# Kernel optimization log

Hardware: AMD Instinct MI355X
Metric: run time of the kernel (lower is better)

## Reference

```python
import jax, jax.numpy as jnp
import numpy as np

B, T, C = 4, 2048, 1024   # batch, seq (block_size), n_embd
H, D = 16, 64             # num_heads, head_size (H*D == C)


def setup_inputs() -> dict:
    key = jax.random.key(0)
    ks = jax.random.split(key, 6)
    s = 0.02
    return {
        "x":  jax.random.normal(ks[0], (B, T, C), jnp.float32),
        "Wq": jax.random.normal(ks[1], (H, C, D), jnp.float32) * s,
        "Wk": jax.random.normal(ks[2], (H, C, D), jnp.float32) * s,
        "Wv": jax.random.normal(ks[3], (H, C, D), jnp.float32) * s,
        "Wp": jax.random.normal(ks[4], (C, C), jnp.float32) * s,
        "bp": jnp.zeros((C,), jnp.float32),
        "is_masked": 1,
    }


def reference(x, Wq, Wk, Wv, Wp, bp, is_masked):
    # Batched per-head projections (original loops over H separate Linears)
    q = jnp.einsum("btc,hcd->bhtd", x, Wq)
    k = jnp.einsum("btc,hcd->bhtd", x, Wk)
    v = jnp.einsum("btc,hcd->bhtd", x, Wv)
    # NOTE: original divides by sqrt(C) where C = n_embd (input dim), not head_size
    scores = jnp.einsum("bhtd,bhsd->bhts", q, k) / jnp.sqrt(jnp.asarray(C, x.dtype))
    if is_masked:
        causal = jnp.tril(jnp.ones((T, T), bool))
        scores = jnp.where(causal, scores, jnp.asarray(-jnp.inf, scores.dtype))
    attn = jax.nn.softmax(scores, axis=-1)   # dropout is identity in eval mode
    out = jnp.einsum("bhts,bhsd->bhtd", attn, v)
    # concat heads along the last dim: [B,T,H*D] == [B,T,C]
    out = out.transpose(0, 2, 1, 3).reshape(B, T, C)
    return out @ Wp.T + bp
```

## Files before the change

kernel.cpp:

```cpp
#include <hip/hip_runtime.h>
#include <stdint.h>
#include <type_traits>

typedef unsigned short u16;
typedef unsigned int u32;
typedef __attribute__((ext_vector_type(8))) short frag8;
typedef __attribute__((ext_vector_type(4))) float fx4;
typedef __attribute__((ext_vector_type(16))) float fx16;

#define MFMA(a, b, c) __builtin_amdgcn_mfma_f32_16x16x32_bf16((a), (b), (c), 0, 0, 0)
#define MFMA32(a, b, c) __builtin_amdgcn_mfma_f32_32x32x16_bf16((a), (b), (c), 0, 0, 0)

__device__ __forceinline__ void gload16(const void* g, void* l) {
  __builtin_amdgcn_global_load_lds((const __attribute__((address_space(1))) void*)g,
                                   (__attribute__((address_space(3))) void*)l, 16, 0, 0);
}

__device__ __forceinline__ u16 f2bf(float f) {
  union { float f; unsigned int u; } c; c.f = f;
  unsigned int r = c.u + 0x7FFFu + ((c.u >> 16) & 1u);
  return (u16)(r >> 16);
}

__device__ __forceinline__ u32 cvtpk(float lo, float hi) {
  u32 r;
  asm("v_cvt_pk_bf16_f32 %0, %1, %2" : "=v"(r) : "v"(lo), "v"(hi));
  return r;
}


__global__ __launch_bounds__(256) void cvt_x(const float* __restrict__ x, u16* __restrict__ xb) {
  const int n4 = (8192 * 1024) / 4;
  for (int i = blockIdx.x * 256 + threadIdx.x; i < n4; i += 2048 * 256) {
    float4 v = ((const float4*)x)[i];
    ushort4 o;
    o.x = f2bf(v.x); o.y = f2bf(v.y); o.z = f2bf(v.z); o.w = f2bf(v.w);
    ((ushort4*)xb)[i] = o;
  }
}

__global__ __launch_bounds__(256) void cvt_wqkv(const float* __restrict__ Wq,
                                                const float* __restrict__ Wk,
                                                const float* __restrict__ Wv,
                                                u16* __restrict__ Wt) {
  __shared__ u16 Tls[64][72];
  int hh = blockIdx.x;
  int c0 = blockIdx.y * 64;
  int type = hh >> 4, h = hh & 15;
  const float* Wsrc = (type == 0 ? Wq : (type == 1 ? Wk : Wv)) + (size_t)h * 1024 * 64;
  int t = threadIdx.x;
  int cr = t >> 4, q4 = (t & 15) * 4;
  for (int i = 0; i < 4; ++i) {
    int c = cr + i * 16;
    float4 v = *(const float4*)(Wsrc + (size_t)(c0 + c) * 64 + q4);
    Tls[q4 + 0][c] = f2bf(v.x);
    Tls[q4 + 1][c] = f2bf(v.y);
    Tls[q4 + 2][c] = f2bf(v.z);
    Tls[q4 + 3][c] = f2bf(v.w);
  }
  __syncthreads();
  for (int i = 0; i < 4; ++i) {
    int d = cr + i * 16;
    ushort4 o;
    o.x = Tls[d][q4 + 0]; o.y = Tls[d][q4 + 1]; o.z = Tls[d][q4 + 2]; o.w = Tls[d][q4 + 3];
    *(ushort4*)(Wt + ((size_t)hh * 64 + d) * 1024 + c0 + q4) = o;
  }
}

__global__ __launch_bounds__(256) void cvt_wp(const float* __restrict__ Wp, u16* __restrict__ wb) {
  const int n4 = (1024 * 1024) / 4;
  for (int i = blockIdx.x * 256 + threadIdx.x; i < n4; i += 1024 * 256) {
    float4 v = ((const float4*)Wp)[i];
    ushort4 o;
    o.x = f2bf(v.x); o.y = f2bf(v.y); o.z = f2bf(v.z); o.w = f2bf(v.w);
    ((ushort4*)wb)[i] = o;
  }
}

__global__ __launch_bounds__(256) void transpose_v(const u16* __restrict__ Vb, u16* __restrict__ VTg) {
  __shared__ u16 T[64 * 64];
  int bh = blockIdx.x, t0 = blockIdx.y * 64;
  const u16* src = Vb + ((size_t)bh * 2048 + t0) * 64;
  int tid = threadIdx.x;
  int tl = tid >> 2, c16 = (tid & 3) * 16;
  int swzw = (tl & 7) << 4;
  frag8 a = *(const frag8*)(src + (size_t)tl * 64 + c16);
  frag8 b = *(const frag8*)(src + (size_t)tl * 64 + c16 + 8);
  *(frag8*)((char*)T + tl * 128 + ((c16 * 2) ^ swzw)) = a;
  *(frag8*)((char*)T + tl * 128 + ((c16 * 2 + 16) ^ swzw)) = b;
  __syncthreads();
  int d_ = tid & 63;
#pragma unroll
  for (int k = 0; k < 2; ++k) {
    int c_ = (tid >> 6) + 4 * k;
    frag8 o;
#pragma unroll
    for (int j = 0; j < 8; ++j) {
      int t = c_ * 8 + j;
      o[j] = *(const u16*)((const char*)T + t * 128 + ((2 * d_) ^ ((t & 7) << 4)));
    }
    *(frag8*)(VTg + ((size_t)bh * 64 + d_) * 2048 + t0 + c_ * 8) = o;
  }
}


template <int BN, int MODE>
__global__ __launch_bounds__(512, 2) void gemm2(const u16* __restrict__ A, const u16* __restrict__ Bw,
                                                u16* __restrict__ Qb, u16* __restrict__ Kb,
                                                u16* __restrict__ Vb, float* __restrict__ outp,
                                                const float* __restrict__ bp) {
  constexpr int NI = BN / 64;
  constexpr int NB = BN / 64;
  constexpr int BBYTES = BN * 128;
  __shared__ __align__(16) char LDSC[65536 + 3 * BBYTES];
  const int tid = threadIdx.x, w = tid >> 6, lane = tid & 63;
  const int lr = lane & 15, lg = lane >> 4;
  constexpr int NBY = (BN == 192) ? 16 : 8;
  const int wg = blockIdx.x;
  const int xcd = wg & 7, loc = wg >> 3;
  const int bx = xcd * 4 + loc / NBY;
  const int by = loc % NBY;
  const int m0 = bx * 256, n0 = by * BN;
  const int r8 = lane >> 3;
  const int c8 = ((lane & 7) ^ r8) * 8;
  const u16* aS[4];
  const u16* bS[NB];
#pragma unroll
  for (int l = 0; l < 4; ++l) aS[l] = A + (size_t)(m0 + l * 64 + w * 8 + r8) * 1024 + c8;
#pragma unroll
  for (int l = 0; l < NB; ++l) bS[l] = Bw + (size_t)(n0 + l * 64 + w * 8 + r8) * 1024 + c8;
  const int wmB = (w >> 2) * 128, wnB = (w & 3) * (BN / 4);

  auto rdA = [&](const char* ab, int mi, int ks) -> frag8 {
    int row = wmB + mi * 16 + lr;
    return *(const frag8*)(ab + row * 128 + ((((ks << 2) + lg) ^ (lr & 7)) << 4));
  };
  auto rdB = [&](const char* bbuf, int ni, int ks) -> frag8 {
    int row = wnB + ni * 16 + lr;
    return *(const frag8*)(bbuf + row * 128 + ((((ks << 2) + lg) ^ (lr & 7)) << 4));
  };

  fx4 acc[8][NI] = {};

#pragma unroll
  for (int l = 0; l < 4; ++l) gload16(aS[l], LDSC + l * 8192 + w * 1024);
#pragma unroll
  for (int l = 0; l < NB; ++l) gload16(bS[l], LDSC + 65536 + l * 8192 + w * 1024);
#pragma unroll
  for (int l = 0; l < NB; ++l) gload16(bS[l] + 64, LDSC + 65536 + BBYTES + l * 8192 + w * 1024);
  if constexpr (NB == 3) asm volatile("s_waitcnt vmcnt(3)" ::: "memory");
  else asm volatile("s_waitcnt vmcnt(2)" ::: "memory");
  __builtin_amdgcn_s_barrier();

  for (int t = 0; t < 16; ++t) {
    const char* ab = LDSC + (t & 1) * 32768;
    const char* bb = LDSC + 65536 + (t % 3) * BBYTES;
    char* abN = LDSC + ((t + 1) & 1) * 32768;
    char* bbN = LDSC + 65536 + ((t + 2) % 3) * BBYTES;
    frag8 bfr[NI][2];
#pragma unroll
    for (int q = 0; q < 4; ++q) {
      if (q == 0) {
#pragma unroll
        for (int ni = 0; ni < NI; ++ni) {
          bfr[ni][0] = rdB(bb, ni, 0);
          bfr[ni][1] = rdB(bb, ni, 1);
        }
      }
      frag8 a00 = rdA(ab, 2 * q + 0, 0), a01 = rdA(ab, 2 * q + 0, 1);
      frag8 a10 = rdA(ab, 2 * q + 1, 0), a11 = rdA(ab, 2 * q + 1, 1);
      if (q == 0 && t + 1 < 16) {
#pragma unroll
        for (int l = 0; l < 4; ++l) gload16(aS[l] + (t + 1) * 64, abN + l * 8192 + w * 1024);
      }
      if (q == 2 && t + 2 < 16) {
        gload16(bS[0] + (t + 2) * 64, bbN + 0 * 8192 + w * 1024);
        gload16(bS[1] + (t + 2) * 64, bbN + 1 * 8192 + w * 1024);
      }
      if (q == 3 && t + 2 < 16 && NB == 3) {
        gload16(bS[2] + (t + 2) * 64, bbN + 2 * 8192 + w * 1024);
      }
      __builtin_amdgcn_s_barrier();
      __builtin_amdgcn_s_setprio(1);
#pragma unroll
      for (int ni = 0; ni < NI; ++ni) {
        acc[2 * q + 0][ni] = MFMA(a00, bfr[ni][0], acc[2 * q + 0][ni]);
        acc[2 * q + 0][ni] = MFMA(a01, bfr[ni][1], acc[2 * q + 0][ni]);
        acc[2 * q + 1][ni] = MFMA(a10, bfr[ni][0], acc[2 * q + 1][ni]);
        acc[2 * q + 1][ni] = MFMA(a11, bfr[ni][1], acc[2 * q + 1][ni]);
      }
      __builtin_amdgcn_s_setprio(0);
      if (q == 3) {
        if (t < 14) {
          if constexpr (NB == 3) asm volatile("s_waitcnt vmcnt(3)" ::: "memory");
          else asm volatile("s_waitcnt vmcnt(2)" ::: "memory");
        } else {
          asm volatile("s_waitcnt vmcnt(0)" ::: "memory");
        }
      }
      __builtin_amdgcn_s_barrier();
    }
  }

#pragma unroll
  for (int mi = 0; mi < 8; ++mi)
#pragma unroll
    for (int r = 0; r < 4; ++r) {
      int m = m0 + wmB + mi * 16 + lg * 4 + r;
      if (MODE == 0) {
        int b = m >> 11, tt = m & 2047;
#pragma unroll
        for (int ni = 0; ni < NI; ++ni) {
          int n = n0 + wnB + ni * 16 + lr;
          int type = n >> 10, h = (n >> 6) & 15, d = n & 63;
          u16* dst = (type == 0) ? Qb : ((type == 1) ? Kb : Vb);
          float v = acc[mi][ni][r];
          if (type == 0) v *= 0.04508422002778011f;
          dst[((size_t)(b * 16 + h) * 2048 + tt) * 64 + d] = f2bf(v);
        }
      } else {
#pragma unroll
        for (int ni = 0; ni < NI; ++ni) {
          int n = n0 + wnB + ni * 16 + lr;
          outp[(size_t)m * 1024 + n] = acc[mi][ni][r] + bp[n];
        }
      }
    }
}


__global__ __launch_bounds__(256, 4) void attn(const u16* __restrict__ Qb, const u16* __restrict__ Kb,
                                               const u16* __restrict__ VTg, u16* __restrict__ Ao,
                                               const int* __restrict__ mflag) {
  __shared__ __align__(16) char LDS[32768];
  const int tid = threadIdx.x, w = tid >> 6, lane = tid & 63;
  const int l31 = lane & 31, hi = lane >> 5;
  const int bh = blockIdx.x;
  const int qt = 15 - (int)blockIdx.y;
  const int masked = mflag[0];
  const int qbase = qt * 128;
  const u16* Qh = Qb + (size_t)bh * (2048 * 64);
  const u16* Kh = Kb + (size_t)bh * (2048 * 64);
  const u16* Vh = VTg + (size_t)bh * (64 * 2048);
  const int qrow = qbase + w * 32 + l31;
  frag8 qf[4];
#pragma unroll
  for (int s = 0; s < 4; ++s) qf[s] = *(const frag8*)(Qh + (size_t)qrow * 64 + s * 16 + hi * 8);
  const int srow = lane >> 3;
  const int schunk = ((lane & 7) ^ srow) * 8;
  const int c0 = w * 2, c1 = w * 2 + 1;
  const u16* kg0 = Kh + (size_t)(c0 * 8 + srow) * 64 + schunk;
  const u16* kg1 = Kh + (size_t)(c1 * 8 + srow) * 64 + schunk;
  const u16* vg0 = Vh + (size_t)(c0 * 8 + srow) * 2048 + schunk;
  const u16* vg1 = Vh + (size_t)(c1 * 8 + srow) * 2048 + schunk;
  const int aK = l31 * 128 + ((hi * 16) ^ ((l31 & 7) << 4));
  const int qmax_w = qbase + w * 32 + 31;
  const int qmin_w = qbase + w * 32;
  float m_run = -__builtin_inff(), l_run = 0.f;
  fx16 oa0 = {}, oa1 = {};
  const int nt = masked ? (2 * qt + 2) : 32;

  auto STAGE = [&](int B, int T) {
    size_t ko = (size_t)T * 4096, vo = (size_t)T * 64;
    gload16(kg0 + ko, LDS + B * 8192 + c0 * 1024);
    gload16(kg1 + ko, LDS + B * 8192 + c1 * 1024);
    gload16(vg0 + vo, LDS + 16384 + B * 8192 + c0 * 1024);
    gload16(vg1 + vo, LDS + 16384 + B * 8192 + c1 * 1024);
  };

  auto TILE = [&](auto Bc, int T) {
    constexpr int B = decltype(Bc)::value;
    if (T + 1 < nt) STAGE(B ^ 1, T + 1);
    bool act = (!masked) || (T * 64 <= qmax_w);
    if (act) {
      fx16 s0v = {}, s1v = {};
#pragma unroll
      for (int ds = 0; ds < 4; ++ds) {
        frag8 k0 = *(const frag8*)(LDS + B * 8192 + (aK ^ (ds << 5)));
        frag8 k1 = *(const frag8*)(LDS + B * 8192 + 4096 + (aK ^ (ds << 5)));
        s0v = MFMA32(k0, qf[ds], s0v);
        s1v = MFMA32(k1, qf[ds], s1v);
      }
      if (masked && T * 64 + 63 > qmin_w) {
#pragma unroll
        for (int g = 0; g < 4; ++g)
#pragma unroll
          for (int r = 0; r < 4; ++r) {
            int sg = T * 64 + r + 8 * g + 4 * hi;
            if (sg > qrow) s0v[4 * g + r] = -__builtin_inff();
            if (sg + 32 > qrow) s1v[4 * g + r] = -__builtin_inff();
          }
      }
      float mx = s0v[0];
#pragma unroll
      for (int i = 1; i < 16; ++i) mx = fmaxf(mx, s0v[i]);
#pragma unroll
      for (int i = 0; i < 16; ++i) mx = fmaxf(mx, s1v[i]);
      mx = fmaxf(mx, __int_as_float(__shfl_xor(__float_as_int(mx), 32)));
      if (!__all(mx <= m_run + 8.0f)) {
        float mn = fmaxf(m_run, mx);
        float al = __builtin_amdgcn_exp2f(m_run - mn);
#pragma unroll
        for (int i = 0; i < 16; ++i) { oa0[i] *= al; oa1[i] *= al; }
        l_run *= al;
        m_run = mn;
      }
      float ps = 0.f;
#pragma unroll
      for (int i = 0; i < 16; ++i) {
        s0v[i] = __builtin_amdgcn_exp2f(s0v[i] - m_run); ps += s0v[i];
      }
#pragma unroll
      for (int i = 0; i < 16; ++i) {
        s1v[i] = __builtin_amdgcn_exp2f(s1v[i] - m_run); ps += s1v[i];
      }
      ps += __int_as_float(__shfl_xor(__float_as_int(ps), 32));
      l_run += ps;
#pragma unroll
      for (int kt = 0; kt < 4; ++kt) {
        const int b8 = (kt & 1) * 8;
        float p0, p1, p2, p3, p4, p5, p6, p7;
        if (kt < 2) { p0=s0v[b8+0];p1=s0v[b8+1];p2=s0v[b8+2];p3=s0v[b8+3];p4=s0v[b8+4];p5=s0v[b8+5];p6=s0v[b8+6];p7=s0v[b8+7]; }
        else        { p0=s1v[b8+0];p1=s1v[b8+1];p2=s1v[b8+2];p3=s1v[b8+3];p4=s1v[b8+4];p5=s1v[b8+5];p6=s1v[b8+6];p7=s1v[b8+7]; }
        u32 X0 = cvtpk(p0, p1), X1 = cvtpk(p2, p3);
        u32 Y0 = cvtpk(p4, p5), Y1 = cvtpk(p6, p7);
        u32 sel0 = hi ? X0 : Y0, sel1 = hi ? X1 : Y1;
        u32 got0 = (u32)__shfl_xor((int)sel0, 32);
        u32 got1 = (u32)__shfl_xor((int)sel1, 32);
        union { u32 u[4]; frag8 f; } pf;
        pf.u[0] = hi ? got0 : X0;
        pf.u[1] = hi ? got1 : X1;
        pf.u[2] = hi ? Y0 : got0;
        pf.u[3] = hi ? Y1 : got1;
        frag8 v0 = *(const frag8*)(LDS + 16384 + B * 8192 + (aK ^ (kt << 5)));
        frag8 v1 = *(const frag8*)(LDS + 16384 + B * 8192 + 4096 + (aK ^ (kt << 5)));
        oa0 = MFMA32(v0, pf.f, oa0);
        oa1 = MFMA32(v1, pf.f, oa1);
      }
    }
    asm volatile("s_waitcnt vmcnt(0)" ::: "memory");
    __builtin_amdgcn_s_barrier();
  };

  STAGE(0, 0);
  asm volatile("s_waitcnt vmcnt(0)" ::: "memory");
  __builtin_amdgcn_s_barrier();
  int t = 0;
  while (true) {
    TILE(std::integral_constant<int, 0>{}, t); ++t; if (t >= nt) break;
    TILE(std::integral_constant<int, 1>{}, t); ++t; if (t >= nt) break;
  }

  float inv = 1.0f / l_run;
  int b = bh >> 4, hh = bh & 15;
  u16* orow = Ao + ((size_t)b * 2048 + qrow) * 1024 + hh * 64;
#pragma unroll
  for (int g = 0; g < 4; ++g) {
    int d0 = 8 * g + 4 * hi;
    u32 wA = cvtpk(oa0[4 * g + 0] * inv, oa0[4 * g + 1] * inv);
    u32 wB = cvtpk(oa0[4 * g + 2] * inv, oa0[4 * g + 3] * inv);
    u32 wC = cvtpk(oa1[4 * g + 0] * inv, oa1[4 * g + 1] * inv);
    u32 wD = cvtpk(oa1[4 * g + 2] * inv, oa1[4 * g + 3] * inv);
    *(u32*)(orow + d0 + 0) = wA;
    *(u32*)(orow + d0 + 2) = wB;
    *(u32*)(orow + d0 + 32) = wC;
    *(u32*)(orow + d0 + 34) = wD;
  }
}


extern "C" void kernel_launch(void* const* d_in, const int* in_sizes, int n_in,
                              void* d_out, int out_size, void* d_ws, size_t ws_size,
                              hipStream_t stream) {
  const float* x = (const float*)d_in[0];
  const float* Wq = (const float*)d_in[1];
  const float* Wk = (const float*)d_in[2];
  const float* Wv = (const float*)d_in[3];
  const float* Wp = (const float*)d_in[4];
  const float* bp = (const float*)d_in[5];
  const int* is_masked = (const int*)d_in[6];
  float* out = (float*)d_out;
  char* ws = (char*)d_ws;
  u16* Xbf = (u16*)(ws + 0);
  u16* Wt  = (u16*)(ws + 16777216);
  u16* Wpb = (u16*)(ws + 23068672);
  u16* Qb  = (u16*)(ws + 25165824);
  u16* Kb  = (u16*)(ws + 41943040);
  u16* Vb  = (u16*)(ws + 58720256);
  u16* Ao  = (u16*)(ws + 75497472);
  u16* VTg = Xbf;

  cvt_x<<<2048, 256, 0, stream>>>(x, Xbf);
  cvt_wqkv<<<dim3(48, 16), 256, 0, stream>>>(Wq, Wk, Wv, Wt);
  cvt_wp<<<1024, 256, 0, stream>>>(Wp, Wpb);
  gemm2<192, 0><<<512, 512, 0, stream>>>(Xbf, Wt, Qb, Kb, Vb, nullptr, nullptr);
  transpose_v<<<dim3(64, 32), 256, 0, stream>>>(Vb, VTg);
  attn<<<dim3(64, 16), 256, 0, stream>>>(Qb, Kb, VTg, Ao, is_masked);
  gemm2<128, 1><<<256, 512, 0, stream>>>(Ao, Wpb, nullptr, nullptr, nullptr, out, bp);
}
```

Measured before the change: 161.2 us.

## Retile GEMM warps to 4x2 layout, single barrier per k-step, tree reductions in softmax

The projection GEMM changes its warp layout from 2x4 (128 rows per warp) to 4x2 (64 rows by BN/2 columns per warp). Each k-step now issues all of its global-to-LDS prefetches up front, software-pipelines the A-fragment reads across the m loop, and uses one barrier per k-step instead of eight. Launch bounds drop to one block per SM to allow more registers. In the attention kernel, the row max and sum reductions become balanced trees to shorten dependency chains. The trade-off is lower occupancy in exchange for fewer barriers and better instruction-level parallelism.

```diff
diff --git a/kernel.cpp b/kernel.cpp
--- a/kernel.cpp
+++ b/kernel.cpp
@@ -26,6 +26,10 @@
   u32 r;
   asm("v_cvt_pk_bf16_f32 %0, %1, %2" : "=v"(r) : "v"(lo), "v"(hi));
   return r;
+}
+
+__device__ __forceinline__ float fmax3(float a, float b, float c) {
+  return fmaxf(fmaxf(a, b), c);
 }
 
 
@@ -105,11 +109,11 @@
 
 
 template <int BN, int MODE>
-__global__ __launch_bounds__(512, 2) void gemm2(const u16* __restrict__ A, const u16* __restrict__ Bw,
+__global__ __launch_bounds__(512, 1) void gemm2(const u16* __restrict__ A, const u16* __restrict__ Bw,
                                                 u16* __restrict__ Qb, u16* __restrict__ Kb,
                                                 u16* __restrict__ Vb, float* __restrict__ outp,
                                                 const float* __restrict__ bp) {
-  constexpr int NI = BN / 64;
+  constexpr int NI = BN / 32;
   constexpr int NB = BN / 64;
   constexpr int BBYTES = BN * 128;
   __shared__ __align__(16) char LDSC[65536 + 3 * BBYTES];
@@ -129,7 +133,7 @@
   for (int l = 0; l < 4; ++l) aS[l] = A + (size_t)(m0 + l * 64 + w * 8 + r8) * 1024 + c8;
 #pragma unroll
   for (int l = 0; l < NB; ++l) bS[l] = Bw + (size_t)(n0 + l * 64 + w * 8 + r8) * 1024 + c8;
-  const int wmB = (w >> 2) * 128, wnB = (w & 3) * (BN / 4);
+  const int wmB = (w >> 1) * 64, wnB = (w & 1) * (BN / 2);
 
   auto rdA = [&](const char* ab, int mi, int ks) -> frag8 {
     int row = wmB + mi * 16 + lr;
@@ -140,7 +144,7 @@
     return *(const frag8*)(bbuf + row * 128 + ((((ks << 2) + lg) ^ (lr & 7)) << 4));
   };
 
-  fx4 acc[8][NI] = {};
+  fx4 acc[4][NI] = {};
 
 #pragma unroll
   for (int l = 0; l < 4; ++l) gload16(aS[l], LDSC + l * 8192 + w * 1024);
@@ -157,53 +161,47 @@
     const char* bb = LDSC + 65536 + (t % 3) * BBYTES;
     char* abN = LDSC + ((t + 1) & 1) * 32768;
     char* bbN = LDSC + 65536 + ((t + 2) % 3) * BBYTES;
-    frag8 bfr[NI][2];
-#pragma unroll
-    for (int q = 0; q < 4; ++q) {
-      if (q == 0) {
-#pragma unroll
-        for (int ni = 0; ni < NI; ++ni) {
-          bfr[ni][0] = rdB(bb, ni, 0);
-          bfr[ni][1] = rdB(bb, ni, 1);
-        }
-      }
-      frag8 a00 = rdA(ab, 2 * q + 0, 0), a01 = rdA(ab, 2 * q + 0, 1);
-      frag8 a10 = rdA(ab, 2 * q + 1, 0), a11 = rdA(ab, 2 * q + 1, 1);
-      if (q == 0 && t + 1 < 16) {
-#pragma unroll
-        for (int l = 0; l < 4; ++l) gload16(aS[l] + (t + 1) * 64, abN + l * 8192 + w * 1024);
-      }
-      if (q == 2 && t + 2 < 16) {
-        gload16(bS[0] + (t + 2) * 64, bbN + 0 * 8192 + w * 1024);
-        gload16(bS[1] + (t + 2) * 64, bbN + 1 * 8192 + w * 1024);
-      }
-      if (q == 3 && t + 2 < 16 && NB == 3) {
-        gload16(bS[2] + (t + 2) * 64, bbN + 2 * 8192 + w * 1024);
-      }
-      __builtin_amdgcn_s_barrier();
+    if (t + 1 < 16) {
+#pragma unroll
+      for (int l = 0; l < 4; ++l) gload16(aS[l] + (t + 1) * 64, abN + l * 8192 + w * 1024);
+    }
+    if (t + 2 < 16) {
+#pragma unroll
+      for (int l = 0; l < NB; ++l) gload16(bS[l] + (t + 2) * 64, bbN + l * 8192 + w * 1024);
+    }
+    frag8 Bf[NI][2];
+#pragma unroll
+    for (int ni = 0; ni < NI; ++ni) {
+      Bf[ni][0] = rdB(bb, ni, 0);
+      Bf[ni][1] = rdB(bb, ni, 1);
+    }
+    frag8 a0 = rdA(ab, 0, 0), a1 = rdA(ab, 0, 1);
+#pragma unroll
+    for (int mi = 0; mi < 4; ++mi) {
+      frag8 c0 = a0, c1 = a1;
+      if (mi < 3) {
+        a0 = rdA(ab, mi + 1, 0);
+        a1 = rdA(ab, mi + 1, 1);
+      }
       __builtin_amdgcn_s_setprio(1);
 #pragma unroll
       for (int ni = 0; ni < NI; ++ni) {
-        acc[2 * q + 0][ni] = MFMA(a00, bfr[ni][0], acc[2 * q + 0][ni]);
-        acc[2 * q + 0][ni] = MFMA(a01, bfr[ni][1], acc[2 * q + 0][ni]);
-        acc[2 * q + 1][ni] = MFMA(a10, bfr[ni][0], acc[2 * q + 1][ni]);
-        acc[2 * q + 1][ni] = MFMA(a11, bfr[ni][1], acc[2 * q + 1][ni]);
+        acc[mi][ni] = MFMA(c0, Bf[ni][0], acc[mi][ni]);
+        acc[mi][ni] = MFMA(c1, Bf[ni][1], acc[mi][ni]);
       }
       __builtin_amdgcn_s_setprio(0);
-      if (q == 3) {
-        if (t < 14) {
-          if constexpr (NB == 3) asm volatile("s_waitcnt vmcnt(3)" ::: "memory");
-          else asm volatile("s_waitcnt vmcnt(2)" ::: "memory");
-        } else {
-          asm volatile("s_waitcnt vmcnt(0)" ::: "memory");
-        }
-      }
-      __builtin_amdgcn_s_barrier();
-    }
-  }
-
-#pragma unroll
-  for (int mi = 0; mi < 8; ++mi)
+    }
+    if (t < 14) {
+      if constexpr (NB == 3) asm volatile("s_waitcnt vmcnt(3)" ::: "memory");
+      else asm volatile("s_waitcnt vmcnt(2)" ::: "memory");
+    } else {
+      asm volatile("s_waitcnt vmcnt(0)" ::: "memory");
+    }
+    __builtin_amdgcn_s_barrier();
+  }
+
+#pragma unroll
+  for (int mi = 0; mi < 4; ++mi)
 #pragma unroll
     for (int r = 0; r < 4; ++r) {
       int m = m0 + wmB + mi * 16 + lg * 4 + r;
@@ -291,11 +289,14 @@
             if (sg + 32 > qrow) s1v[4 * g + r] = -__builtin_inff();
           }
       }
-      float mx = s0v[0];
-#pragma unroll
-      for (int i = 1; i < 16; ++i) mx = fmaxf(mx, s0v[i]);
-#pragma unroll
-      for (int i = 0; i < 16; ++i) mx = fmaxf(mx, s1v[i]);
+      float tmx[8];
+#pragma unroll
+      for (int i = 0; i < 8; ++i)
+        tmx[i] = fmaxf(fmaxf(s0v[i], s0v[i + 8]), fmaxf(s1v[i], s1v[i + 8]));
+      float r0 = fmax3(tmx[0], tmx[1], tmx[2]);
+      float r1 = fmax3(tmx[3], tmx[4], tmx[5]);
+      float r2 = fmax3(tmx[6], tmx[7], r0);
+      float mx = fmaxf(r1, r2);
       mx = fmaxf(mx, __int_as_float(__shfl_xor(__float_as_int(mx), 32)));
       if (!__all(mx <= m_run + 8.0f)) {
         float mn = fmaxf(m_run, mx);
@@ -305,15 +306,17 @@
         l_run *= al;
         m_run = mn;
       }
-      float ps = 0.f;
-#pragma unroll
-      for (int i = 0; i < 16; ++i) {
-        s0v[i] = __builtin_amdgcn_exp2f(s0v[i] - m_run); ps += s0v[i];
-      }
-#pragma unroll
-      for (int i = 0; i < 16; ++i) {
-        s1v[i] = __builtin_amdgcn_exp2f(s1v[i] - m_run); ps += s1v[i];
-      }
+#pragma unroll
+      for (int i = 0; i < 16; ++i) s0v[i] = __builtin_amdgcn_exp2f(s0v[i] - m_run);
+#pragma unroll
+      for (int i = 0; i < 16; ++i) s1v[i] = __builtin_amdgcn_exp2f(s1v[i] - m_run);
+      float tps[8];
+#pragma unroll
+      for (int i = 0; i < 8; ++i)
+        tps[i] = (s0v[i] + s0v[i + 8]) + (s1v[i] + s1v[i + 8]);
+      float u0 = (tps[0] + tps[1]) + (tps[2] + tps[3]);
+      float u1 = (tps[4] + tps[5]) + (tps[6] + tps[7]);
+      float ps = u0 + u1;
       ps += __int_as_float(__shfl_xor(__float_as_int(ps), 32));
       l_run += ps;
 #pragma unroll
```

New measurement: 161.8 us. About the same (+0.4%).
